# Kernel tuning notes

Measured on AMD Instinct MI355X. Metric: run time of the kernel, lower is better.

Reference implementation:

```python
import jax, jax.numpy as jnp
import numpy as np

PART_INDICES = [[0, 1, 2, 3, 4], [5, 6, 11, 12], [5, 7, 9], [6, 8, 10], [11, 12, 13, 14, 15, 16]]
B, J, D_IN, D_H, D_OUT = 4096, 25, 512, 256, 512


def _xavier(key, shape):
    fan_in, fan_out = shape
    lim = float(np.sqrt(6.0 / (fan_in + fan_out)))
    return jax.random.uniform(key, shape, jnp.float32, -lim, lim)


def setup_inputs() -> dict:
    key = jax.random.key(0)
    ks = list(jax.random.split(key, 64))
    it = iter(ks)
    inp = {}
    inp["x"] = jax.random.normal(next(it), (B, J, D_IN), jnp.float32)
    inp["adj_global"] = jax.random.uniform(next(it), (J, J), jnp.float32)
    for p, idx in enumerate(PART_INDICES):
        n = len(idx)
        inp[f"adj_local_{p}"] = jax.random.uniform(next(it), (n, n), jnp.float32)
    # global GCN params (2 layers)
    inp["Wg0"] = _xavier(next(it), (D_IN, D_H)); inp["bg0"] = jnp.zeros((D_H,), jnp.float32)
    inp["Wg1"] = _xavier(next(it), (D_H, D_OUT)); inp["bg1"] = jnp.zeros((D_OUT,), jnp.float32)
    # local GCN params (5 parts x 2 layers)
    for p in range(5):
        inp[f"Wl{p}a"] = _xavier(next(it), (D_IN, D_H)); inp[f"bl{p}a"] = jnp.zeros((D_H,), jnp.float32)
        inp[f"Wl{p}b"] = _xavier(next(it), (D_H, D_OUT)); inp[f"bl{p}b"] = jnp.zeros((D_OUT,), jnp.float32)
    # fusion MLP: Linear(2*D_OUT, D_OUT) -> ReLU -> Linear(D_OUT, D_OUT)
    inp["Wf0"] = _xavier(next(it), (2 * D_OUT, D_OUT)); inp["bf0"] = jnp.zeros((D_OUT,), jnp.float32)
    inp["Wf1"] = _xavier(next(it), (D_OUT, D_OUT)); inp["bf1"] = jnp.zeros((D_OUT,), jnp.float32)
    return inp


def _gcn(x, adj, W, b):
    # symmetric degree normalization D^-1/2 A D^-1/2, then (norm_adj @ (x @ W)) + b
    d = jnp.clip(adj.sum(axis=1), 1e-6, None) ** -0.5
    norm_adj = d[:, None] * adj * d[None, :]                       # [n, n]
    return jnp.einsum('ij,bjf->bif', norm_adj, x @ W) + b          # [B, n, out]


def reference(x, adj_global, adj_local_0, adj_local_1, adj_local_2, adj_local_3, adj_local_4,
              Wg0, bg0, Wg1, bg1,
              Wl0a, bl0a, Wl0b, bl0b,
              Wl1a, bl1a, Wl1b, bl1b,
              Wl2a, bl2a, Wl2b, bl2b,
              Wl3a, bl3a, Wl3b, bl3b,
              Wl4a, bl4a, Wl4b, bl4b,
              Wf0, bf0, Wf1, bf1):
    adjs = [adj_local_0, adj_local_1, adj_local_2, adj_local_3, adj_local_4]
    lps = [(Wl0a, bl0a, Wl0b, bl0b), (Wl1a, bl1a, Wl1b, bl1b), (Wl2a, bl2a, Wl2b, bl2b),
           (Wl3a, bl3a, Wl3b, bl3b), (Wl4a, bl4a, Wl4b, bl4b)]
    # global branch
    xg = jax.nn.relu(_gcn(x, adj_global, Wg0, bg0))
    xg = jax.nn.relu(_gcn(xg, adj_global, Wg1, bg1))
    # local branch: scatter per-part outputs back (later parts overwrite overlaps, like torch)
    xl = jnp.zeros((x.shape[0], x.shape[1], D_OUT), x.dtype)
    for p, idx in enumerate(PART_INDICES):
        Wa, ba, Wb, bb = lps[p]
        idx_a = jnp.asarray(idx)
        xp = x[:, idx_a]                                           # [B, n_p, D_IN]
        xp = jax.nn.relu(_gcn(xp, adjs[p], Wa, ba))
        xp = jax.nn.relu(_gcn(xp, adjs[p], Wb, bb))
        xl = xl.at[:, idx_a].set(xp)
    # fusion MLP
    xc = jnp.concatenate([xg, xl], axis=-1)                        # [B, J, 2*D_OUT]
    return jax.nn.relu(xc @ Wf0 + bf0) @ Wf1 + bf1                 # [B, J, D_OUT]
```

## Files before the change

### kernel.cpp

```cpp
#include <hip/hip_runtime.h>


#define BATCH 4096
#define NJOINT 25
#define MROWS (BATCH * NJOINT)
#define SZ_FULL (MROWS * 512)

typedef __attribute__((ext_vector_type(8))) short short8;
typedef __attribute__((ext_vector_type(4))) float float4_;

__device__ __forceinline__ float b2f(ushort u) {
    union { float f; uint32_t i; } x; x.i = ((uint32_t)u) << 16; return x.f;
}
__device__ __forceinline__ ushort f2b(float f) {
    union { float f; uint32_t i; } x; x.f = f;
    uint32_t r = x.i + 0x7fff + ((x.i >> 16) & 1);
    return (ushort)(r >> 16);
}
__device__ __forceinline__ void async16(const void* g, void* l) {
    __builtin_amdgcn_global_load_lds(
        (const __attribute__((address_space(1))) void*)g,
        (__attribute__((address_space(3))) void*)l, 16, 0, 0);
}

__device__ void norm_one(const float* A, int n, float* out, float* sAdj, float* sD) {
    int t = threadIdx.x;
    for (int i = t; i < n * n; i += 256) sAdj[i] = A[i];
    __syncthreads();
    if (t < n) {
        float s = 0.f;
        for (int j = 0; j < n; j++) s += sAdj[t * n + j];
        sD[t] = 1.0f / sqrtf(fmaxf(s, 1e-6f));
    }
    __syncthreads();
    for (int i = t; i < n * n; i += 256) {
        int r = i / n, c = i % n;
        out[i] = sD[r] * sAdj[i] * sD[c];
    }
    __syncthreads();
}

__global__ __launch_bounds__(256) void adjnorm_kernel(
    const float* Ag, const float* A0, const float* A2, const float* A3,
    const float* A4, float* ADJ) {
    __shared__ float sAdj[640];
    __shared__ float sD[32];
    norm_one(Ag, 25, ADJ, sAdj, sD);
    norm_one(A0, 5, ADJ + 640 + 0 * 64, sAdj, sD);
    norm_one(A2, 3, ADJ + 640 + 1 * 64, sAdj, sD);
    norm_one(A3, 3, ADJ + 640 + 2 * 64, sAdj, sD);
    norm_one(A4, 6, ADJ + 640 + 3 * 64, sAdj, sD);
}

__global__ __launch_bounds__(256) void cvt_bf16(const float* __restrict__ in,
                                                ushort* __restrict__ out, int n4) {
    int id = blockIdx.x * 256 + threadIdx.x;
    if (id < n4) {
        float4 v = ((const float4*)in)[id];
        ushort4 o;
        o.x = f2b(v.x); o.y = f2b(v.y); o.z = f2b(v.z); o.w = f2b(v.w);
        ((ushort4*)out)[id] = o;
    }
}

__global__ __launch_bounds__(256) void wtrans(const float* __restrict__ W,
                                              ushort* __restrict__ Wt, int K, int N) {
    __shared__ float tile[32][33];
    int t = threadIdx.x;
    int tx = t & 31, ty = t >> 5;
    int k0 = blockIdx.y * 32, n0 = blockIdx.x * 32;
    for (int r = ty; r < 32; r += 8)
        tile[r][tx] = W[(size_t)(k0 + r) * N + n0 + tx];
    __syncthreads();
    for (int r = ty; r < 32; r += 8)
        Wt[(size_t)(n0 + r) * K + k0 + tx] = f2b(tile[tx][r]);
}

__global__ __launch_bounds__(256) void zero_tail(ushort* __restrict__ XL) {
    int id = blockIdx.x * 256 + threadIdx.x;
    int f4 = id & 127;
    int rj = (id >> 7) & 7;
    int b = id >> 10;
    ushort4 z; z.x = 0; z.y = 0; z.z = 0; z.w = 0;
    ((ushort4*)(XL + ((size_t)(b * 25 + 17 + rj) * 512)))[f4] = z;
}

template <bool GATHER, bool CONCAT, bool BIAS, bool RELU, bool OUTF32>
__global__ __launch_bounds__(256) void mfma_gemm(
    const ushort* __restrict__ A, const ushort* __restrict__ A2,
    const ushort* __restrict__ Wt, const float* __restrict__ bias,
    void* __restrict__ C, int M, int N, int K, int lda,
    int gn, int g0, int g1, int g2, int g3, int g4, int g5) {
    __shared__ ushort As[128][32];
    __shared__ ushort Bs[128][32];
    int t = threadIdx.x;
    int w = t >> 6;
    int l = t & 63;
    int bm = blockIdx.y * 128, bn = blockIdx.x * 128;

    int sr0 = bm + (w << 4) + (l >> 2);
    int sr1 = sr0 + 64;
    int wr0 = bn + (w << 4) + (l >> 2);
    int wr1 = wr0 + 64;
    if (GATHER) {
        int b0 = sr0 / gn, j0 = sr0 - b0 * gn;
        int b1 = sr1 / gn, j1 = sr1 - b1 * gn;
        int map[6] = {g0, g1, g2, g3, g4, g5};
        sr0 = b0 * 25 + map[j0];
        sr1 = b1 * 25 + map[j1];
    }
    int ch = (l & 3) * 8;

    float4_ acc[4][4];
#pragma unroll
    for (int i = 0; i < 4; i++)
#pragma unroll
        for (int j = 0; j < 4; j++) acc[i][j] = (float4_)0.f;

    int wm = w >> 1, wn = w & 1;
    int lr = l & 15;
    int qk = (l >> 4) * 8;

    for (int k0 = 0; k0 < K; k0 += 32) {
        const ushort *a0, *a1;
        if (CONCAT) {
            const ushort* src = (k0 < 512) ? A : A2;
            int ko = k0 & 511;
            a0 = src + (size_t)sr0 * 512 + ko + ch;
            a1 = src + (size_t)sr1 * 512 + ko + ch;
        } else {
            a0 = A + (size_t)sr0 * lda + k0 + ch;
            a1 = A + (size_t)sr1 * lda + k0 + ch;
        }
        const ushort* b0 = Wt + (size_t)wr0 * K + k0 + ch;
        const ushort* b1 = Wt + (size_t)wr1 * K + k0 + ch;
        async16(a0, &As[(w << 4)][0]);
        async16(a1, &As[64 + (w << 4)][0]);
        async16(b0, &Bs[(w << 4)][0]);
        async16(b1, &Bs[64 + (w << 4)][0]);
        __syncthreads();

        short8 af[4], bf[4];
#pragma unroll
        for (int i = 0; i < 4; i++)
            af[i] = *(const short8*)&As[(wm << 6) + i * 16 + lr][qk];
#pragma unroll
        for (int j = 0; j < 4; j++)
            bf[j] = *(const short8*)&Bs[(wn << 6) + j * 16 + lr][qk];
#pragma unroll
        for (int i = 0; i < 4; i++)
#pragma unroll
            for (int j = 0; j < 4; j++)
                acc[i][j] = __builtin_amdgcn_mfma_f32_16x16x32_bf16(
                    af[i], bf[j], acc[i][j], 0, 0, 0);
        __syncthreads();
    }

    int quad = l >> 4, cl = l & 15;
#pragma unroll
    for (int j = 0; j < 4; j++) {
        int col = bn + (wn << 6) + j * 16 + cl;
        float bv = BIAS ? bias[col] : 0.f;
#pragma unroll
        for (int i = 0; i < 4; i++) {
#pragma unroll
            for (int r = 0; r < 4; r++) {
                int row = bm + (wm << 6) + i * 16 + (quad << 2) + r;
                float v = acc[i][j][r] + bv;
                if (RELU) v = fmaxf(v, 0.f);
                if (OUTF32)
                    ((float*)C)[(size_t)row * N + col] = v;
                else
                    ((ushort*)C)[(size_t)row * N + col] = f2b(v);
            }
        }
    }
}

template <int NJ>
__global__ __launch_bounds__(256) void mix_inplace(
    ushort* __restrict__ T, const float* __restrict__ adjn,
    const float* __restrict__ bias, int F) {
    __shared__ float As[NJ * NJ];
    int t = threadIdx.x;
    for (int i = t; i < NJ * NJ; i += 256) As[i] = adjn[i];
    __syncthreads();
    int id = blockIdx.x * 256 + t;
    int f = id % F;
    int b = id / F;
    ushort* base = T + (size_t)(b * NJ) * F + f;
    float v[NJ];
#pragma unroll
    for (int j = 0; j < NJ; j++) v[j] = b2f(base[(size_t)j * F]);
    float bi = bias[f];
#pragma unroll
    for (int i = 0; i < NJ; i++) {
        float o = 0.f;
#pragma unroll
        for (int j = 0; j < NJ; j++) o += As[i * NJ + j] * v[j];
        base[(size_t)i * F] = f2b(fmaxf(o + bi, 0.f));
    }
}

template <int NJ>
__global__ __launch_bounds__(256) void mix_scatter(
    const ushort* __restrict__ P, const float* __restrict__ adjn,
    const float* __restrict__ bias, ushort* __restrict__ XL,
    int j0, int j1, int j2, int j3, int j4, int j5) {
    __shared__ float As[NJ * NJ];
    __shared__ int jm[NJ];
    int t = threadIdx.x;
    for (int i = t; i < NJ * NJ; i += 256) As[i] = adjn[i];
    if (t == 0) {
        int tmp[6] = {j0, j1, j2, j3, j4, j5};
        for (int i = 0; i < NJ; i++) jm[i] = tmp[i];
    }
    __syncthreads();
    int id = blockIdx.x * 256 + t;
    int f = id & 511;
    int b = id >> 9;
    float v[NJ];
    const ushort* base = P + (size_t)(b * NJ) * 512 + f;
#pragma unroll
    for (int j = 0; j < NJ; j++) v[j] = b2f(base[(size_t)j * 512]);
    float bi = bias[f];
#pragma unroll
    for (int i = 0; i < NJ; i++) {
        float o = 0.f;
#pragma unroll
        for (int j = 0; j < NJ; j++) o += As[i * NJ + j] * v[j];
        XL[((size_t)(b * 25 + jm[i])) * 512 + f] = f2b(fmaxf(o + bi, 0.f));
    }
}

extern "C" void kernel_launch(void* const* d_in, const int* in_sizes, int n_in,
                              void* d_out, int out_size, void* d_ws,
                              size_t ws_size, hipStream_t stream) {
    const float* x    = (const float*)d_in[0];
    const float* adjg = (const float*)d_in[1];
    const float* al0  = (const float*)d_in[2];
    const float* al2  = (const float*)d_in[4];
    const float* al3  = (const float*)d_in[5];
    const float* al4  = (const float*)d_in[6];
    const float* Wg0  = (const float*)d_in[7];
    const float* bg0  = (const float*)d_in[8];
    const float* Wg1  = (const float*)d_in[9];
    const float* bg1  = (const float*)d_in[10];
    const float* Wf0  = (const float*)d_in[31];
    const float* bf0  = (const float*)d_in[32];
    const float* Wf1  = (const float*)d_in[33];
    const float* bf1  = (const float*)d_in[34];

    float* ws = (float*)d_ws;
    float* ADJ = ws;
    ushort* U  = (ushort*)(ws + 4096);
    ushort* Xb = U;
    ushort* XG = U + (size_t)SZ_FULL;
    ushort* XL = U + (size_t)2 * SZ_FULL;
    ushort* S  = U + (size_t)3 * SZ_FULL;
    ushort* T  = S;
    ushort* P1 = S;
    ushort* P3 = S + 6291456;
    ushort* Wb = S + 26214400;
    ushort* HF = Xb;

    ushort* Wg0t = Wb;
    ushort* Wg1t = Wb + 131072;
    ushort* Wf0t = Wb + 1310720;
    ushort* Wf1t = Wb + 1835008;

    dim3 blk(256);

    adjnorm_kernel<<<1, blk, 0, stream>>>(adjg, al0, al2, al3, al4, ADJ);
    cvt_bf16<<<SZ_FULL / 4 / 256, blk, 0, stream>>>(x, Xb, SZ_FULL / 4);
    zero_tail<<<16384, blk, 0, stream>>>(XL);

    wtrans<<<dim3(256 / 32, 512 / 32), blk, 0, stream>>>(Wg0, Wg0t, 512, 256);
    wtrans<<<dim3(512 / 32, 256 / 32), blk, 0, stream>>>(Wg1, Wg1t, 256, 512);
    wtrans<<<dim3(512 / 32, 1024 / 32), blk, 0, stream>>>(Wf0, Wf0t, 1024, 512);
    wtrans<<<dim3(512 / 32, 512 / 32), blk, 0, stream>>>(Wf1, Wf1t, 512, 512);

    struct Part { int n, widx; int idx[6]; };
    const Part parts[4] = {
        {5, 11, {0, 1, 2, 3, 4, 0}},
        {3, 19, {5, 7, 9, 0, 0, 0}},
        {3, 23, {6, 8, 10, 0, 0, 0}},
        {6, 27, {11, 12, 13, 14, 15, 16}},
    };
    for (int q = 0; q < 4; q++) {
        ushort* Wat = Wb + 262144 + q * 262144;
        ushort* Wbt = Wat + 131072;
        wtrans<<<dim3(8, 16), blk, 0, stream>>>((const float*)d_in[parts[q].widx], Wat, 512, 256);
        wtrans<<<dim3(16, 8), blk, 0, stream>>>((const float*)d_in[parts[q].widx + 2], Wbt, 256, 512);
    }

    mfma_gemm<false, false, false, false, false><<<dim3(2, 800), blk, 0, stream>>>(
        Xb, nullptr, Wg0t, nullptr, T, MROWS, 256, 512, 512, 0, 0, 0, 0, 0, 0, 0);
    mix_inplace<25><<<BATCH * 256 / 256, blk, 0, stream>>>(T, ADJ, bg0, 256);
    mfma_gemm<false, false, false, false, false><<<dim3(4, 800), blk, 0, stream>>>(
        T, nullptr, Wg1t, nullptr, XG, MROWS, 512, 256, 256, 0, 0, 0, 0, 0, 0, 0);
    mix_inplace<25><<<BATCH * 512 / 256, blk, 0, stream>>>(XG, ADJ, bg1, 512);

    const int slots[4] = {0, 1, 2, 3};
    for (int q = 0; q < 4; q++) {
        const Part& P = parts[q];
        const float* ba = (const float*)d_in[P.widx + 1];
        const float* bb = (const float*)d_in[P.widx + 3];
        ushort* Wat = Wb + 262144 + q * 262144;
        ushort* Wbt = Wat + 131072;
        const float* adjl = ADJ + 640 + slots[q] * 64;
        int M = BATCH * P.n;
        mfma_gemm<true, false, false, false, false><<<dim3(2, M / 128), blk, 0, stream>>>(
            Xb, nullptr, Wat, nullptr, P1, M, 256, 512, 512,
            P.n, P.idx[0], P.idx[1], P.idx[2], P.idx[3], P.idx[4], P.idx[5]);
        if (P.n == 5)
            mix_inplace<5><<<BATCH * 256 / 256, blk, 0, stream>>>(P1, adjl, ba, 256);
        else if (P.n == 3)
            mix_inplace<3><<<BATCH * 256 / 256, blk, 0, stream>>>(P1, adjl, ba, 256);
        else
            mix_inplace<6><<<BATCH * 256 / 256, blk, 0, stream>>>(P1, adjl, ba, 256);
        mfma_gemm<false, false, false, false, false><<<dim3(4, M / 128), blk, 0, stream>>>(
            P1, nullptr, Wbt, nullptr, P3, M, 512, 256, 256, 0, 0, 0, 0, 0, 0, 0);
        if (P.n == 5)
            mix_scatter<5><<<BATCH * 512 / 256, blk, 0, stream>>>(
                P3, adjl, bb, XL, P.idx[0], P.idx[1], P.idx[2], P.idx[3], P.idx[4], P.idx[5]);
        else if (P.n == 3)
            mix_scatter<3><<<BATCH * 512 / 256, blk, 0, stream>>>(
                P3, adjl, bb, XL, P.idx[0], P.idx[1], P.idx[2], P.idx[3], P.idx[4], P.idx[5]);
        else
            mix_scatter<6><<<BATCH * 512 / 256, blk, 0, stream>>>(
                P3, adjl, bb, XL, P.idx[0], P.idx[1], P.idx[2], P.idx[3], P.idx[4], P.idx[5]);
    }

    mfma_gemm<false, true, true, true, false><<<dim3(4, 800), blk, 0, stream>>>(
        XG, XL, Wf0t, bf0, HF, MROWS, 512, 1024, 1024, 0, 0, 0, 0, 0, 0, 0);
    mfma_gemm<false, false, true, false, true><<<dim3(4, 800), blk, 0, stream>>>(
        HF, nullptr, Wf1t, bf1, (float*)d_out, MROWS, 512, 512, 512, 0, 0, 0, 0, 0, 0, 0);

    (void)in_sizes; (void)n_in; (void)out_size; (void)ws_size;
}
```

Baseline: 1.118 ms.

## Replace GEMM with 256x256-tile pipelined MFMA kernel and interleaved concat buffer

Swaps the 128x128 single-buffered MFMA GEMM for a 256x256-tile, 512-thread kernel. It adds a 4-slot async LDS ring with prefetch two stages ahead, XOR-swizzled LDS layout, XCD-aware block remapping, and raised wave priority around the MFMA block. The global and local branch outputs now go into one interleaved [M,1024] buffer, so the fusion GEMM reads a contiguous K=1024 row instead of branching between two sources. It aims to raise arithmetic reuse and hide load latency, at the cost of 128KB of LDS per block and large accumulator register pressure. Small-M local GEMMs may see fewer blocks.

```diff
diff --git a/kernel.cpp b/kernel.cpp
--- a/kernel.cpp
+++ b/kernel.cpp
@@ -76,111 +76,141 @@
         Wt[(size_t)(n0 + r) * K + k0 + tx] = f2b(tile[tx][r]);
 }
 
-__global__ __launch_bounds__(256) void zero_tail(ushort* __restrict__ XL) {
+__global__ __launch_bounds__(256) void zero_tail(ushort* __restrict__ XGL) {
     int id = blockIdx.x * 256 + threadIdx.x;
     int f4 = id & 127;
     int rj = (id >> 7) & 7;
     int b = id >> 10;
     ushort4 z; z.x = 0; z.y = 0; z.z = 0; z.w = 0;
-    ((ushort4*)(XL + ((size_t)(b * 25 + 17 + rj) * 512)))[f4] = z;
-}
-
-template <bool GATHER, bool CONCAT, bool BIAS, bool RELU, bool OUTF32>
-__global__ __launch_bounds__(256) void mfma_gemm(
-    const ushort* __restrict__ A, const ushort* __restrict__ A2,
-    const ushort* __restrict__ Wt, const float* __restrict__ bias,
-    void* __restrict__ C, int M, int N, int K, int lda,
+    ((ushort4*)(XGL + ((size_t)(b * 25 + 17 + rj) * 1024 + 512)))[f4] = z;
+}
+
+template <bool GATHER, bool BIAS, bool RELU, bool OUTF32>
+__global__ __launch_bounds__(512, 2) void gemm256(
+    const ushort* __restrict__ A, const ushort* __restrict__ Wt,
+    const float* __restrict__ bias, void* __restrict__ C,
+    int M, int N, int K, int lda, int ldc,
     int gn, int g0, int g1, int g2, int g3, int g4, int g5) {
-    __shared__ ushort As[128][32];
-    __shared__ ushort Bs[128][32];
-    int t = threadIdx.x;
-    int w = t >> 6;
-    int l = t & 63;
-    int bm = blockIdx.y * 128, bn = blockIdx.x * 128;
-
-    int sr0 = bm + (w << 4) + (l >> 2);
-    int sr1 = sr0 + 64;
-    int wr0 = bn + (w << 4) + (l >> 2);
-    int wr1 = wr0 + 64;
+    __shared__ ushort lds[65536];
+    int t = threadIdx.x;
+    int l = t & 63, w = t >> 6;
+
+    int nwg = (int)gridDim.x;
+    int cpx = nwg >> 3;
+    int wg = ((int)blockIdx.x & 7) * cpx + ((int)blockIdx.x >> 3);
+    int gx = N >> 8;
+    int tm = wg / gx, tn = wg - tm * gx;
+    int bm = tm << 8, bn = tn << 8;
+
+    int rA0 = (w << 4) + (l >> 2);
+    int rA1 = 128 + rA0;
+    int qp = l & 3;
+    int qA0 = qp ^ ((rA0 >> 1) & 3);
+    int qA1 = qp ^ ((rA1 >> 1) & 3);
+    int grA0 = bm + rA0, grA1 = bm + rA1;
     if (GATHER) {
-        int b0 = sr0 / gn, j0 = sr0 - b0 * gn;
-        int b1 = sr1 / gn, j1 = sr1 - b1 * gn;
         int map[6] = {g0, g1, g2, g3, g4, g5};
-        sr0 = b0 * 25 + map[j0];
-        sr1 = b1 * 25 + map[j1];
-    }
-    int ch = (l & 3) * 8;
-
-    float4_ acc[4][4];
-#pragma unroll
-    for (int i = 0; i < 4; i++)
-#pragma unroll
-        for (int j = 0; j < 4; j++) acc[i][j] = (float4_)0.f;
-
-    int wm = w >> 1, wn = w & 1;
-    int lr = l & 15;
-    int qk = (l >> 4) * 8;
-
-    for (int k0 = 0; k0 < K; k0 += 32) {
-        const ushort *a0, *a1;
-        if (CONCAT) {
-            const ushort* src = (k0 < 512) ? A : A2;
-            int ko = k0 & 511;
-            a0 = src + (size_t)sr0 * 512 + ko + ch;
-            a1 = src + (size_t)sr1 * 512 + ko + ch;
+        int b0 = grA0 / gn; grA0 = b0 * 25 + map[grA0 - b0 * gn];
+        int b1 = grA1 / gn; grA1 = b1 * 25 + map[grA1 - b1 * gn];
+    }
+    const ushort* pA0 = A + (size_t)grA0 * lda + (qA0 << 3);
+    const ushort* pA1 = A + (size_t)grA1 * lda + (qA1 << 3);
+    const ushort* pB0 = Wt + (size_t)(bn + rA0) * K + (qA0 << 3);
+    const ushort* pB1 = Wt + (size_t)(bn + rA1) * K + (qA1 << 3);
+    int sA0 = w << 9;
+    int sA1 = (8 + w) << 9;
+
+    int wm = w >> 2, wn = w & 3;
+    int lr = l & 15, q = l >> 4;
+    int aoff[8], boff[4];
+#pragma unroll
+    for (int fi = 0; fi < 8; fi++) {
+        int r = (wm << 7) + (fi << 4) + lr;
+        aoff[fi] = (r << 5) + ((q ^ ((r >> 1) & 3)) << 3);
+    }
+#pragma unroll
+    for (int fj = 0; fj < 4; fj++) {
+        int r = (wn << 6) + (fj << 4) + lr;
+        boff[fj] = 8192 + (r << 5) + ((q ^ ((r >> 1) & 3)) << 3);
+    }
+
+    float4_ acc[8][4];
+#pragma unroll
+    for (int fi = 0; fi < 8; fi++)
+#pragma unroll
+        for (int fj = 0; fj < 4; fj++) acc[fi][fj] = (float4_)0.f;
+
+    int NT = K >> 5;
+
+#define STAGE(kt_) do {                                      \
+        int bo_ = ((kt_) & 3) << 14;                         \
+        int ko_ = (kt_) << 5;                                \
+        async16(pA0 + ko_, &lds[bo_ + sA0]);                 \
+        async16(pA1 + ko_, &lds[bo_ + sA1]);                 \
+        async16(pB0 + ko_, &lds[bo_ + 8192 + sA0]);          \
+        async16(pB1 + ko_, &lds[bo_ + 8192 + sA1]);          \
+    } while (0)
+
+    STAGE(0);
+    STAGE(1);
+    for (int kt = 0; kt < NT; ++kt) {
+        if (kt + 2 < NT) {
+            STAGE(kt + 2);
+            asm volatile("s_waitcnt vmcnt(8)" ::: "memory");
+        } else if (kt + 1 < NT) {
+            asm volatile("s_waitcnt vmcnt(4)" ::: "memory");
         } else {
-            a0 = A + (size_t)sr0 * lda + k0 + ch;
-            a1 = A + (size_t)sr1 * lda + k0 + ch;
+            asm volatile("s_waitcnt vmcnt(0)" ::: "memory");
         }
-        const ushort* b0 = Wt + (size_t)wr0 * K + k0 + ch;
-        const ushort* b1 = Wt + (size_t)wr1 * K + k0 + ch;
-        async16(a0, &As[(w << 4)][0]);
-        async16(a1, &As[64 + (w << 4)][0]);
-        async16(b0, &Bs[(w << 4)][0]);
-        async16(b1, &Bs[64 + (w << 4)][0]);
-        __syncthreads();
-
-        short8 af[4], bf[4];
-#pragma unroll
-        for (int i = 0; i < 4; i++)
-            af[i] = *(const short8*)&As[(wm << 6) + i * 16 + lr][qk];
-#pragma unroll
-        for (int j = 0; j < 4; j++)
-            bf[j] = *(const short8*)&Bs[(wn << 6) + j * 16 + lr][qk];
-#pragma unroll
-        for (int i = 0; i < 4; i++)
-#pragma unroll
-            for (int j = 0; j < 4; j++)
-                acc[i][j] = __builtin_amdgcn_mfma_f32_16x16x32_bf16(
-                    af[i], bf[j], acc[i][j], 0, 0, 0);
-        __syncthreads();
-    }
-
-    int quad = l >> 4, cl = l & 15;
-#pragma unroll
-    for (int j = 0; j < 4; j++) {
-        int col = bn + (wn << 6) + j * 16 + cl;
-        float bv = BIAS ? bias[col] : 0.f;
-#pragma unroll
-        for (int i = 0; i < 4; i++) {
-#pragma unroll
-            for (int r = 0; r < 4; r++) {
-                int row = bm + (wm << 6) + i * 16 + (quad << 2) + r;
-                float v = acc[i][j][r] + bv;
+        __builtin_amdgcn_s_barrier();
+        __builtin_amdgcn_sched_barrier(0);
+        int bo = (kt & 3) << 14;
+        short8 af[8], bf[4];
+#pragma unroll
+        for (int fj = 0; fj < 4; fj++) bf[fj] = *(const short8*)&lds[bo + boff[fj]];
+#pragma unroll
+        for (int fi = 0; fi < 8; fi++) af[fi] = *(const short8*)&lds[bo + aoff[fi]];
+        __builtin_amdgcn_s_setprio(1);
+#pragma unroll
+        for (int fi = 0; fi < 8; fi++)
+#pragma unroll
+            for (int fj = 0; fj < 4; fj++)
+                acc[fi][fj] = __builtin_amdgcn_mfma_f32_16x16x32_bf16(
+                    af[fi], bf[fj], acc[fi][fj], 0, 0, 0);
+        __builtin_amdgcn_s_setprio(0);
+    }
+#undef STAGE
+
+    int cl = lr;
+    float bv[4];
+#pragma unroll
+    for (int fj = 0; fj < 4; fj++)
+        bv[fj] = BIAS ? bias[bn + (wn << 6) + (fj << 4) + cl] : 0.f;
+#pragma unroll
+    for (int fi = 0; fi < 8; fi++) {
+        int row0 = bm + (wm << 7) + (fi << 4) + (q << 2);
+#pragma unroll
+        for (int r = 0; r < 4; r++) {
+            size_t rowoff = (size_t)(row0 + r) * ldc;
+#pragma unroll
+            for (int fj = 0; fj < 4; fj++) {
+                int col = bn + (wn << 6) + (fj << 4) + cl;
+                float v = acc[fi][fj][r] + bv[fj];
                 if (RELU) v = fmaxf(v, 0.f);
                 if (OUTF32)
-                    ((float*)C)[(size_t)row * N + col] = v;
+                    ((float*)C)[rowoff + col] = v;
                 else
-                    ((ushort*)C)[(size_t)row * N + col] = f2b(v);
+                    ((ushort*)C)[rowoff + col] = f2b(v);
             }
         }
     }
+    (void)M;
 }
 
 template <int NJ>
 __global__ __launch_bounds__(256) void mix_inplace(
     ushort* __restrict__ T, const float* __restrict__ adjn,
-    const float* __restrict__ bias, int F) {
+    const float* __restrict__ bias, int F, int ldr) {
     __shared__ float As[NJ * NJ];
     int t = threadIdx.x;
     for (int i = t; i < NJ * NJ; i += 256) As[i] = adjn[i];
@@ -188,17 +218,17 @@
     int id = blockIdx.x * 256 + t;
     int f = id % F;
     int b = id / F;
-    ushort* base = T + (size_t)(b * NJ) * F + f;
+    ushort* base = T + (size_t)(b * NJ) * ldr + f;
     float v[NJ];
 #pragma unroll
-    for (int j = 0; j < NJ; j++) v[j] = b2f(base[(size_t)j * F]);
+    for (int j = 0; j < NJ; j++) v[j] = b2f(base[(size_t)j * ldr]);
     float bi = bias[f];
 #pragma unroll
     for (int i = 0; i < NJ; i++) {
         float o = 0.f;
 #pragma unroll
         for (int j = 0; j < NJ; j++) o += As[i * NJ + j] * v[j];
-        base[(size_t)i * F] = f2b(fmaxf(o + bi, 0.f));
+        base[(size_t)i * ldr] = f2b(fmaxf(o + bi, 0.f));
     }
 }
 
@@ -229,7 +259,7 @@
         float o = 0.f;
 #pragma unroll
         for (int j = 0; j < NJ; j++) o += As[i * NJ + j] * v[j];
-        XL[((size_t)(b * 25 + jm[i])) * 512 + f] = f2b(fmaxf(o + bi, 0.f));
+        XL[((size_t)(b * 25 + jm[i])) * 1024 + f] = f2b(fmaxf(o + bi, 0.f));
     }
 }
 
@@ -254,10 +284,9 @@
     float* ws = (float*)d_ws;
     float* ADJ = ws;
     ushort* U  = (ushort*)(ws + 4096);
-    ushort* Xb = U;
-    ushort* XG = U + (size_t)SZ_FULL;
-    ushort* XL = U + (size_t)2 * SZ_FULL;
-    ushort* S  = U + (size_t)3 * SZ_FULL;
+    ushort* Xb  = U;
+    ushort* XGL = U + (size_t)SZ_FULL;
+    ushort* S   = XGL + (size_t)MROWS * 1024;
     ushort* T  = S;
     ushort* P1 = S;
     ushort* P3 = S + 6291456;
@@ -270,10 +299,11 @@
     ushort* Wf1t = Wb + 1835008;
 
     dim3 blk(256);
+    dim3 blk512(512);
 
     adjnorm_kernel<<<1, blk, 0, stream>>>(adjg, al0, al2, al3, al4, ADJ);
     cvt_bf16<<<SZ_FULL / 4 / 256, blk, 0, stream>>>(x, Xb, SZ_FULL / 4);
-    zero_tail<<<16384, blk, 0, stream>>>(XL);
+    zero_tail<<<16384, blk, 0, stream>>>(XGL);
 
     wtrans<<<dim3(256 / 32, 512 / 32), blk, 0, stream>>>(Wg0, Wg0t, 512, 256);
     wtrans<<<dim3(512 / 32, 256 / 32), blk, 0, stream>>>(Wg1, Wg1t, 256, 512);
@@ -294,12 +324,12 @@
         wtrans<<<dim3(16, 8), blk, 0, stream>>>((const float*)d_in[parts[q].widx + 2], Wbt, 256, 512);
     }
 
-    mfma_gemm<false, false, false, false, false><<<dim3(2, 800), blk, 0, stream>>>(
-        Xb, nullptr, Wg0t, nullptr, T, MROWS, 256, 512, 512, 0, 0, 0, 0, 0, 0, 0);
-    mix_inplace<25><<<BATCH * 256 / 256, blk, 0, stream>>>(T, ADJ, bg0, 256);
-    mfma_gemm<false, false, false, false, false><<<dim3(4, 800), blk, 0, stream>>>(
-        T, nullptr, Wg1t, nullptr, XG, MROWS, 512, 256, 256, 0, 0, 0, 0, 0, 0, 0);
-    mix_inplace<25><<<BATCH * 512 / 256, blk, 0, stream>>>(XG, ADJ, bg1, 512);
+    gemm256<false, false, false, false><<<400, blk512, 0, stream>>>(
+        Xb, Wg0t, nullptr, T, MROWS, 256, 512, 512, 256, 0, 0, 0, 0, 0, 0, 0);
+    mix_inplace<25><<<BATCH * 256 / 256, blk, 0, stream>>>(T, ADJ, bg0, 256, 256);
+    gemm256<false, false, false, false><<<800, blk512, 0, stream>>>(
+        T, Wg1t, nullptr, XGL, MROWS, 512, 256, 256, 1024, 0, 0, 0, 0, 0, 0, 0);
+    mix_inplace<25><<<BATCH * 512 / 256, blk, 0, stream>>>(XGL, ADJ, bg1, 512, 1024);
 
     const int slots[4] = {0, 1, 2, 3};
     for (int q = 0; q < 4; q++) {
@@ -310,32 +340,32 @@
         ushort* Wbt = Wat + 131072;
         const float* adjl = ADJ + 640 + slots[q] * 64;
         int M = BATCH * P.n;
-        mfma_gemm<true, false, false, false, false><<<dim3(2, M / 128), blk, 0, stream>>>(
-            Xb, nullptr, Wat, nullptr, P1, M, 256, 512, 512,
+        gemm256<true, false, false, false><<<M / 256, blk512, 0, stream>>>(
+            Xb, Wat, nullptr, P1, M, 256, 512, 512, 256,
             P.n, P.idx[0], P.idx[1], P.idx[2], P.idx[3], P.idx[4], P.idx[5]);
         if (P.n == 5)
-            mix_inplace<5><<<BATCH * 256 / 256, blk, 0, stream>>>(P1, adjl, ba, 256);
+            mix_inplace<5><<<BATCH * 256 / 256, blk, 0, stream>>>(P1, adjl, ba, 256, 256);
         else if (P.n == 3)
-            mix_inplace<3><<<BATCH * 256 / 256, blk, 0, stream>>>(P1, adjl, ba, 256);
+            mix_inplace<3><<<BATCH * 256 / 256, blk, 0, stream>>>(P1, adjl, ba, 256, 256);
         else
-            mix_inplace<6><<<BATCH * 256 / 256, blk, 0, stream>>>(P1, adjl, ba, 256);
-        mfma_gemm<false, false, false, false, false><<<dim3(4, M / 128), blk, 0, stream>>>(
-            P1, nullptr, Wbt, nullptr, P3, M, 512, 256, 256, 0, 0, 0, 0, 0, 0, 0);
+            mix_inplace<6><<<BATCH * 256 / 256, blk, 0, stream>>>(P1, adjl, ba, 256, 256);
+        gemm256<false, false, false, false><<<(M / 256) * 2, blk512, 0, stream>>>(
+            P1, Wbt, nullptr, P3, M, 512, 256, 256, 512, 0, 0, 0, 0, 0, 0, 0);
         if (P.n == 5)
             mix_scatter<5><<<BATCH * 512 / 256, blk, 0, stream>>>(
-                P3, adjl, bb, XL, P.idx[0], P.idx[1], P.idx[2], P.idx[3], P.idx[4], P.idx[5]);
+                P3, adjl, bb, XGL + 512, P.idx[0], P.idx[1], P.idx[2], P.idx[3], P.idx[4], P.idx[5]);
         else if (P.n == 3)
             mix_scatter<3><<<BATCH * 512 / 256, blk, 0, stream>>>(
-                P3, adjl, bb, XL, P.idx[0], P.idx[1], P.idx[2], P.idx[3], P.idx[4], P.idx[5]);
+                P3, adjl, bb, XGL + 512, P.idx[0], P.idx[1], P.idx[2], P.idx[3], P.idx[4], P.idx[5]);
         else
             mix_scatter<6><<<BATCH * 512 / 256, blk, 0, stream>>>(
-                P3, adjl, bb, XL, P.idx[0], P.idx[1], P.idx[2], P.idx[3], P.idx[4], P.idx[5]);
-    }
-
-    mfma_gemm<false, true, true, true, false><<<dim3(4, 800), blk, 0, stream>>>(
-        XG, XL, Wf0t, bf0, HF, MROWS, 512, 1024, 1024, 0, 0, 0, 0, 0, 0, 0);
-    mfma_gemm<false, false, true, false, true><<<dim3(4, 800), blk, 0, stream>>>(
-        HF, nullptr, Wf1t, bf1, (float*)d_out, MROWS, 512, 512, 512, 0, 0, 0, 0, 0, 0, 0);
+                P3, adjl, bb, XGL + 512, P.idx[0], P.idx[1], P.idx[2], P.idx[3], P.idx[4], P.idx[5]);
+    }
+
+    gemm256<false, true, true, false><<<800, blk512, 0, stream>>>(
+        XGL, Wf0t, bf0, HF, MROWS, 512, 1024, 1024, 512, 0, 0, 0, 0, 0, 0, 0);
+    gemm256<false, true, false, true><<<800, blk512, 0, stream>>>(
+        HF, Wf1t, bf1, (float*)d_out, MROWS, 512, 512, 512, 512, 0, 0, 0, 0, 0, 0, 0);
 
     (void)in_sizes; (void)n_in; (void)out_size; (void)ws_size;
 }
```

Result: faster. 1.055 ms (-5.7%).
